# Performance work log

Measured on AMD Instinct MI355X. Metric: run time of the kernel, lower is better.

Reference implementation:

```python
import jax, jax.numpy as jnp
import numpy as np

B, C_IN, C_OUT, H, K = 64, 64, 128, 1855, 6


def setup_inputs() -> dict:
    key = jax.random.key(0)
    k1, k2, k3, k4 = jax.random.split(key, 4)
    x = jax.random.normal(k1, (B, C_IN, H), dtype=jnp.float32)
    # neighbor table [H, K]; valid indices first, -1 padding at the end
    neighbors = jax.random.randint(k2, (H, K), 0, H)
    n_boundary = H // 10
    neighbors = neighbors.at[:n_boundary, K - 2:].set(-1)
    weight_center = jax.random.normal(k3, (C_OUT, C_IN), dtype=jnp.float32) / np.sqrt(C_IN).astype(np.float32)
    weight_neighbors = jax.random.normal(k4, (C_OUT, C_IN, K), dtype=jnp.float32) / np.sqrt(C_IN * K).astype(np.float32)
    bias = jnp.zeros((C_OUT,), dtype=jnp.float32)
    return {
        "x": x,
        "neighbors": neighbors,
        "weight_center": weight_center,
        "weight_neighbors": weight_neighbors,
        "bias": bias,
    }


def reference(x, neighbors, weight_center, weight_neighbors, bias):
    # x: [B, C_in, H]; neighbors: [H, K] with -1 = invalid (valid-first ordering)
    mask = neighbors >= 0                               # [H, K]
    idx = jnp.where(mask, neighbors, 0)                 # safe gather indices
    gathered = x[:, :, idx] * mask.astype(x.dtype)[None, None, :, :]  # [B, C_in, H, K]
    center = jnp.einsum('bch,oc->boh', x, weight_center)              # [B, C_out, H]
    neigh = jnp.einsum('bchk,ock->boh', gathered, weight_neighbors)   # [B, C_out, H]
    counts = (1 + mask.sum(axis=-1)).astype(x.dtype)                  # [H]
    return (center + neigh) / counts[None, None, :] + bias[None, :, None]
```

## Files before the change

### kernel.cpp

```cpp
#include <hip/hip_runtime.h>
#include <stdint.h>

typedef __bf16 bf16x8 __attribute__((ext_vector_type(8)));
typedef float floatx4 __attribute__((ext_vector_type(4)));
typedef float floatx4u __attribute__((ext_vector_type(4), aligned(4)));
typedef unsigned int u32x4 __attribute__((ext_vector_type(4)));
typedef unsigned short u16;
typedef unsigned short u16x8 __attribute__((ext_vector_type(8)));
typedef unsigned int u32;

#define CIN   64
#define COUT  128
#define H_    1855
#define KNB   6
#define KTOT  448
#define NSTEPS 14

#define HROW   1040
#define HBUFSZ 16640

#define WP_OFF     ((size_t)H_ * 4096 * 2)
#define CINV_OFF   (WP_OFF + (size_t)COUT * KTOT * 2)
#define ZERO_OFF   (CINV_OFF + 7424)
#define SRCOFF_OFF (ZERO_OFF + 1024)
#define INVOFF 0xFFFFFFFFu

#define PIN4(v) asm volatile("" : "+v"(v))

typedef __attribute__((address_space(1))) unsigned int as1_u32;
typedef __attribute__((address_space(3))) unsigned int as3_u32;
static __device__ __forceinline__ void ld16_to_lds(const void* g, void* l) {
    __builtin_amdgcn_global_load_lds((const as1_u32*)g, (as3_u32*)l, 16, 0, 0);
}

static __device__ inline u16 f32_to_bf16(float f) {
    u32 u = __float_as_uint(f);
    u32 r = (u + 0x7FFFu + ((u >> 16) & 1u)) >> 16;
    return (u16)r;
}

__global__ __launch_bounds__(256) void k_prep(const float* __restrict__ x,
                                              const float* __restrict__ wc,
                                              const float* __restrict__ wn,
                                              const int* __restrict__ nbr,
                                              u16* __restrict__ xt3,
                                              u16* __restrict__ wp,
                                              float* __restrict__ cInvG,
                                              u32* __restrict__ zeroPg,
                                              u32* __restrict__ srcOff) {
    int tid = threadIdx.x;
    if (blockIdx.y == 64) {
        for (int tg = blockIdx.x * 256 + tid; tg < COUT * KTOT; tg += 29 * 256) {
            if (tg < 64) zeroPg[tg] = 0u;
            if (tg < H_) {
                int cnt = 1;
#pragma unroll
                for (int j = 0; j < KNB; ++j) cnt += (nbr[tg * KNB + j] >= 0) ? 1 : 0;
                cInvG[tg] = 1.0f / (float)cnt;
            }
            if (tg < H_ * 8) {
                int h = tg >> 3, s = tg & 7;
                u32 e;
                if (s == 0) e = (u32)h * 8192u;
                else if (s <= 6) {
                    int n = nbr[h * KNB + (s - 1)];
                    e = (n >= 0) ? (u32)n * 8192u : INVOFF;
                } else e = INVOFF;
                srcOff[tg] = e;
            }
            int o = tg / KTOT;
            int rem = tg - o * KTOT;
            int s = rem >> 6, c = rem & 63;
            float v = (s == 0) ? wc[o * CIN + c]
                               : wn[(o * CIN + c) * KNB + (s - 1)];
            wp[tg] = f32_to_bf16(v);
        }
        return;
    }
    __shared__ u16 tile[64][65];
    int h0  = blockIdx.x * 64;
    int bc0 = blockIdx.y * 64;
    int lh   = tid & 15;
    int rowi = tid >> 4;
    bool safe = (h0 + 64 <= H_);
#pragma unroll
    for (int i = 0; i < 4; ++i) {
        int row = i * 16 + rowi;
        int h = h0 + lh * 4;
        u16 v4[4];
        if (safe) {
            floatx4u f = *(const floatx4u*)(x + (size_t)(bc0 + row) * H_ + h);
#pragma unroll
            for (int j = 0; j < 4; ++j) v4[j] = f32_to_bf16(f[j]);
        } else {
#pragma unroll
            for (int j = 0; j < 4; ++j) {
                int hh = h + j;
                v4[j] = (hh < H_) ? f32_to_bf16(x[(size_t)(bc0 + row) * H_ + hh]) : (u16)0;
            }
        }
#pragma unroll
        for (int j = 0; j < 4; ++j) tile[row][lh * 4 + j] = v4[j];
    }
    __syncthreads();
    int bg = tid & 7;
    int hb = tid >> 3;
#pragma unroll
    for (int ii = 0; ii < 2; ++ii) {
        int hl = ii * 32 + hb;
        int hh = h0 + hl;
        u16x8 v;
#pragma unroll
        for (int j = 0; j < 8; ++j) v[j] = tile[bg * 8 + j][hl];
        if (hh < H_)
            *(u16x8*)(xt3 + (size_t)hh * 4096 + bc0 + bg * 8) = v;
    }
}

__global__ __launch_bounds__(256, 2) void k_main(const u16* __restrict__ xt3,
                                                 const u16* __restrict__ wp,
                                                 const float* __restrict__ bias,
                                                 const float* __restrict__ cInvG,
                                                 const u32* __restrict__ srcOff,
                                                 float* __restrict__ out) {
    __shared__ __align__(16) char LDS[4 * HBUFSZ];

    int tid  = threadIdx.x;
    int gbl  = blockIdx.x;
    int bp   = gbl & 31;
    int hs   = gbl >> 5;
    int b0   = bp * 2;
    int h0   = hs * 64;

    int lane = tid & 63;
    int wave = tid >> 6;
    int col  = lane & 15;
    int quad = lane >> 4;
    int m0w  = wave * 32;
    int lane16 = lane & 15;
    int ssub = lane >> 4;
    int bl   = lane16 >> 3;
    int chunk = lane16 & 7;

    const char* xb = (const char*)xt3;

    u32x4 afrag[2][NSTEPS];
#pragma unroll
    for (int mt = 0; mt < 2; ++mt) {
        int o = m0w + mt * 16 + col;
#pragma unroll
        for (int kk = 0; kk < NSTEPS; ++kk)
            afrag[mt][kk] = *(const u32x4*)(wp + o * KTOT + kk * 32 + quad * 8);
    }
#pragma unroll
    for (int mt = 0; mt < 2; ++mt)
#pragma unroll
        for (int kk = 0; kk < NSTEPS; ++kk)
            PIN4(afrag[mt][kk]);

    float biasv[2][4];
#pragma unroll
    for (int mt = 0; mt < 2; ++mt)
#pragma unroll
        for (int r = 0; r < 4; ++r)
            biasv[mt][r] = bias[m0w + mt * 16 + quad * 4 + r];

    float icv[4];
#pragma unroll
    for (int t = 0; t < 4; ++t) {
        int hic = h0 + t * 16 + col;
        icv[t] = cInvG[hic < H_ ? hic : 0];
    }

    u32 colOff = (u32)((b0 + bl) * 128 + chunk * 16);
    u32 zOff   = (u32)ZERO_OFF + (u32)(lane16 * 16);
    u32 offs[4][2][4];
#pragma unroll
    for (int t = 0; t < 4; ++t)
#pragma unroll
        for (int sg = 0; sg < 2; ++sg)
#pragma unroll
            for (int i = 0; i < 4; ++i) {
                int hh = h0 + t * 16 + wave * 4 + i;
                int s  = sg * 4 + ssub;
                u32 e = (hh < H_) ? srcOff[hh * 8 + s] : INVOFF;
                offs[t][sg][i] = (e == INVOFF) ? zOff : (e + colOff);
            }

    int rb0 = col * HROW + quad * 16;
    int rb1 = rb0 + 128;
    char* bufA0 = LDS;
    char* bufA1 = LDS + HBUFSZ;
    char* bufA2 = LDS + 2 * HBUFSZ;
    char* bufA3 = LDS + 3 * HBUFSZ;
    bool bnd = (hs == 28);

#define SGH(t, sg, bufp) do {                                                 \
    char* _d = (bufp) + (wave * 4) * HROW;                                    \
    _Pragma("unroll")                                                         \
    for (int _i = 0; _i < 4; ++_i)                                            \
        ld16_to_lds(xb + offs[t][sg][_i], _d + _i * HROW);                    \
} while (0)

#define CA(accv, bufp) do {                      \
    _Pragma("unroll") for (int _m = 0; _m < 2; ++_m)                          \
    _Pragma("unroll") for (int _n = 0; _n < 2; ++_n)                          \
        accv[_m][_n] = (floatx4){0.0f, 0.0f, 0.0f, 0.0f};                     \
    __builtin_amdgcn_s_setprio(1);                                            \
    _Pragma("unroll")                                                         \
    for (int kk = 0; kk < 8; ++kk) {                                          \
        int koff = (kk >> 1) * 256 + (kk & 1) * 64;                           \
        bf16x8 bfa = *(const bf16x8*)((bufp) + rb0 + koff);                   \
        bf16x8 bfb = *(const bf16x8*)((bufp) + rb1 + koff);                   \
        bf16x8 a0 = __builtin_bit_cast(bf16x8, afrag[0][kk]);                 \
        bf16x8 a1 = __builtin_bit_cast(bf16x8, afrag[1][kk]);                 \
        accv[0][0] = __builtin_amdgcn_mfma_f32_16x16x32_bf16(a0, bfa, accv[0][0], 0, 0, 0); \
        accv[1][0] = __builtin_amdgcn_mfma_f32_16x16x32_bf16(a1, bfa, accv[1][0], 0, 0, 0); \
        accv[0][1] = __builtin_amdgcn_mfma_f32_16x16x32_bf16(a0, bfb, accv[0][1], 0, 0, 0); \
        accv[1][1] = __builtin_amdgcn_mfma_f32_16x16x32_bf16(a1, bfb, accv[1][1], 0, 0, 0); \
    }                                                                         \
    __builtin_amdgcn_s_setprio(0);                                            \
} while (0)

#define CB(accv, bufp) do {                    \
    __builtin_amdgcn_s_setprio(1);                                            \
    _Pragma("unroll")                                                         \
    for (int kk = 8; kk < 14; ++kk) {                                         \
        int koff = ((kk - 8) >> 1) * 256 + (kk & 1) * 64;                     \
        bf16x8 bfa = *(const bf16x8*)((bufp) + rb0 + koff);                   \
        bf16x8 bfb = *(const bf16x8*)((bufp) + rb1 + koff);                   \
        bf16x8 a0 = __builtin_bit_cast(bf16x8, afrag[0][kk]);                 \
        bf16x8 a1 = __builtin_bit_cast(bf16x8, afrag[1][kk]);                 \
        accv[0][0] = __builtin_amdgcn_mfma_f32_16x16x32_bf16(a0, bfa, accv[0][0], 0, 0, 0); \
        accv[1][0] = __builtin_amdgcn_mfma_f32_16x16x32_bf16(a1, bfa, accv[1][0], 0, 0, 0); \
        accv[0][1] = __builtin_amdgcn_mfma_f32_16x16x32_bf16(a0, bfb, accv[0][1], 0, 0, 0); \
        accv[1][1] = __builtin_amdgcn_mfma_f32_16x16x32_bf16(a1, bfb, accv[1][1], 0, 0, 0); \
    }                                                                         \
    __builtin_amdgcn_s_setprio(0);                                            \
} while (0)

#define EPI(pp, a0v, a1v, Ebuf, BND) do {                                     \
    float* _E = (float*)((Ebuf) + (wave * 4) * HROW);                         \
    int _o8 = lane >> 3, _h4 = lane & 7;                                      \
    _Pragma("unroll")                                                         \
    for (int _nt = 0; _nt < 2; ++_nt) {                                       \
        asm volatile("s_waitcnt lgkmcnt(0)" ::: "memory");                    \
        _Pragma("unroll") for (int _mt = 0; _mt < 2; ++_mt)                   \
        _Pragma("unroll") for (int _r = 0; _r < 4; ++_r) {                    \
            int _ol = _mt * 16 + quad * 4 + _r;                               \
            int _x0 = ((col >> 2) ^ (_ol & 7));                               \
            int _x1 = (((16 + col) >> 2) ^ (_ol & 7));                        \
            _E[_ol * 32 + (_x0 << 2) + (col & 3)] =                           \
                a0v[_mt][_nt][_r] * icv[(pp) * 2]     + biasv[_mt][_r];       \
            _E[_ol * 32 + (_x1 << 2) + (col & 3)] =                           \
                a1v[_mt][_nt][_r] * icv[(pp) * 2 + 1] + biasv[_mt][_r];       \
        }                                                                     \
        asm volatile("s_waitcnt lgkmcnt(0)" ::: "memory");                    \
        _Pragma("unroll")                                                     \
        for (int _q = 0; _q < 4; ++_q) {                                      \
            int _ol = _q * 8 + _o8;                                           \
            floatx4 _v = *(const floatx4*)(_E + _ol * 32 + ((_h4 ^ (_ol & 7)) << 2)); \
            int _hh = h0 + (pp) * 32 + _h4 * 4;                               \
            float* _dst = out + (size_t)(b0 + _nt) * ((size_t)COUT * H_)      \
                        + (size_t)(m0w + _ol) * H_ + _hh;                     \
            if (!(BND)) {                                                     \
                *(floatx4u*)_dst = _v;                                        \
            } else {                                                          \
                _Pragma("unroll") for (int _e = 0; _e < 4; ++_e)              \
                    if (_hh + _e < H_) _dst[_e] = _v[_e];                     \
            }                                                                 \
        }                                                                     \
    }                                                                         \
} while (0)

#define VW(n)  asm volatile("s_waitcnt vmcnt(" #n ") lgkmcnt(0)" ::: "memory")
#define BAR()  __builtin_amdgcn_s_barrier()

    floatx4 acc0[2][2], acc1[2][2];

    SGH(0, 0, bufA0);
    SGH(0, 1, bufA1);
    SGH(1, 0, bufA2);

    VW(8);  BAR(); SGH(1, 1, bufA3);  CA(acc0, bufA0);
    VW(8);  BAR(); SGH(2, 0, bufA0);  CB(acc0, bufA1);
    VW(8);  BAR(); SGH(2, 1, bufA1);  CA(acc1, bufA2);
    VW(8);  BAR();                    CB(acc1, bufA3);
    EPI(0, acc0, acc1, bufA2, false);
    VW(12); BAR(); SGH(3, 0, bufA2);  CA(acc0, bufA0);
    VW(12); BAR(); SGH(3, 1, bufA3);  CB(acc0, bufA1);
    VW(4);  BAR();                    CA(acc1, bufA2);
    VW(0);  BAR();                    CB(acc1, bufA3);
    EPI(1, acc0, acc1, bufA2, bnd);

#undef SGH
#undef CA
#undef CB
#undef EPI
#undef VW
#undef BAR
}

extern "C" void kernel_launch(void* const* d_in, const int* in_sizes, int n_in,
                              void* d_out, int out_size, void* d_ws, size_t ws_size,
                              hipStream_t stream) {
    const float* x    = (const float*)d_in[0];
    const int*   nbr  = (const int*)d_in[1];
    const float* wc   = (const float*)d_in[2];
    const float* wn   = (const float*)d_in[3];
    const float* bias = (const float*)d_in[4];

    u16*   xt3    = (u16*)d_ws;
    u16*   wp     = (u16*)((char*)d_ws + WP_OFF);
    float* cInvG  = (float*)((char*)d_ws + CINV_OFF);
    u32*   zeroPg = (u32*)((char*)d_ws + ZERO_OFF);
    u32*   srcOff = (u32*)((char*)d_ws + SRCOFF_OFF);

    k_prep<<<dim3(29, 65), dim3(256), 0, stream>>>(
        x, wc, wn, nbr, xt3, wp, cInvG, zeroPg, srcOff);
    k_main<<<dim3(928), dim3(256), 0, stream>>>(
        xt3, wp, bias, cInvG, srcOff, (float*)d_out);
}
```

Measured before the change: 130.5 us.

## Halve LDS buffering for higher occupancy, write epilogue directly, pack prep transpose

The main kernel now uses two LDS gather buffers instead of four and raises the launch-bounds minimum to 4 blocks per SM, trading pipeline depth (waits now drain to vmcnt 0 at each step) for more resident waves. The epilogue drops its LDS-staged transpose and writes accumulator lanes straight to global memory, sending out-of-range tail writes to a dump buffer instead of branching. The prep transpose packs two bf16 rows per 32-bit LDS word so reads and stores are wider. The risks are less latency hiding per block and scattered, uncoalesced scalar output stores.

```diff
diff --git a/kernel.cpp b/kernel.cpp
--- a/kernel.cpp
+++ b/kernel.cpp
@@ -6,7 +6,6 @@
 typedef float floatx4u __attribute__((ext_vector_type(4), aligned(4)));
 typedef unsigned int u32x4 __attribute__((ext_vector_type(4)));
 typedef unsigned short u16;
-typedef unsigned short u16x8 __attribute__((ext_vector_type(8)));
 typedef unsigned int u32;
 
 #define CIN   64
@@ -23,6 +22,7 @@
 #define CINV_OFF   (WP_OFF + (size_t)COUT * KTOT * 2)
 #define ZERO_OFF   (CINV_OFF + 7424)
 #define SRCOFF_OFF (ZERO_OFF + 1024)
+#define DUMP_OFF   (SRCOFF_OFF + 59392)
 #define INVOFF 0xFFFFFFFFu
 
 #define PIN4(v) asm volatile("" : "+v"(v))
@@ -77,30 +77,36 @@
         }
         return;
     }
-    __shared__ u16 tile[64][65];
+    __shared__ u32 t32[64][34];
     int h0  = blockIdx.x * 64;
     int bc0 = blockIdx.y * 64;
-    int lh   = tid & 15;
-    int rowi = tid >> 4;
+    int lh = tid & 15;
+    int rq = tid >> 4;
     bool safe = (h0 + 64 <= H_);
 #pragma unroll
-    for (int i = 0; i < 4; ++i) {
-        int row = i * 16 + rowi;
+    for (int it = 0; it < 2; ++it) {
+        int rp = it * 16 + rq;
+        size_t r0 = (size_t)(bc0 + rp * 2) * H_;
+        size_t r1 = r0 + H_;
         int h = h0 + lh * 4;
-        u16 v4[4];
+        u32 p[4];
         if (safe) {
-            floatx4u f = *(const floatx4u*)(x + (size_t)(bc0 + row) * H_ + h);
-#pragma unroll
-            for (int j = 0; j < 4; ++j) v4[j] = f32_to_bf16(f[j]);
+            floatx4u f0 = *(const floatx4u*)(x + r0 + h);
+            floatx4u f1 = *(const floatx4u*)(x + r1 + h);
+#pragma unroll
+            for (int j = 0; j < 4; ++j)
+                p[j] = (u32)f32_to_bf16(f0[j]) | ((u32)f32_to_bf16(f1[j]) << 16);
         } else {
 #pragma unroll
             for (int j = 0; j < 4; ++j) {
                 int hh = h + j;
-                v4[j] = (hh < H_) ? f32_to_bf16(x[(size_t)(bc0 + row) * H_ + hh]) : (u16)0;
+                u16 a = 0, b = 0;
+                if (hh < H_) { a = f32_to_bf16(x[r0 + hh]); b = f32_to_bf16(x[r1 + hh]); }
+                p[j] = (u32)a | ((u32)b << 16);
             }
         }
 #pragma unroll
-        for (int j = 0; j < 4; ++j) tile[row][lh * 4 + j] = v4[j];
+        for (int j = 0; j < 4; ++j) t32[lh * 4 + j][rp] = p[j];
     }
     __syncthreads();
     int bg = tid & 7;
@@ -109,21 +115,22 @@
     for (int ii = 0; ii < 2; ++ii) {
         int hl = ii * 32 + hb;
         int hh = h0 + hl;
-        u16x8 v;
-#pragma unroll
-        for (int j = 0; j < 8; ++j) v[j] = tile[bg * 8 + j][hl];
+        uint2 qa = *(const uint2*)&t32[hl][bg * 4];
+        uint2 qb = *(const uint2*)&t32[hl][bg * 4 + 2];
+        u32x4 q = {qa.x, qa.y, qb.x, qb.y};
         if (hh < H_)
-            *(u16x8*)(xt3 + (size_t)hh * 4096 + bc0 + bg * 8) = v;
-    }
-}
-
-__global__ __launch_bounds__(256, 2) void k_main(const u16* __restrict__ xt3,
+            *(u32x4*)(xt3 + (size_t)hh * 4096 + bc0 + bg * 8) = q;
+    }
+}
+
+__global__ __launch_bounds__(256, 4) void k_main(const u16* __restrict__ xt3,
                                                  const u16* __restrict__ wp,
                                                  const float* __restrict__ bias,
                                                  const float* __restrict__ cInvG,
                                                  const u32* __restrict__ srcOff,
+                                                 float* __restrict__ dump,
                                                  float* __restrict__ out) {
-    __shared__ __align__(16) char LDS[4 * HBUFSZ];
+    __shared__ __align__(16) char LDS[2 * HBUFSZ];
 
     int tid  = threadIdx.x;
     int gbl  = blockIdx.x;
@@ -189,10 +196,8 @@
 
     int rb0 = col * HROW + quad * 16;
     int rb1 = rb0 + 128;
-    char* bufA0 = LDS;
-    char* bufA1 = LDS + HBUFSZ;
-    char* bufA2 = LDS + 2 * HBUFSZ;
-    char* bufA3 = LDS + 3 * HBUFSZ;
+    char* buf0 = LDS;
+    char* buf1 = LDS + HBUFSZ;
     bool bnd = (hs == 28);
 
 #define SGH(t, sg, bufp) do {                                                 \
@@ -239,37 +244,19 @@
     __builtin_amdgcn_s_setprio(0);                                            \
 } while (0)
 
-#define EPI(pp, a0v, a1v, Ebuf, BND) do {                                     \
-    float* _E = (float*)((Ebuf) + (wave * 4) * HROW);                         \
-    int _o8 = lane >> 3, _h4 = lane & 7;                                      \
-    _Pragma("unroll")                                                         \
-    for (int _nt = 0; _nt < 2; ++_nt) {                                       \
-        asm volatile("s_waitcnt lgkmcnt(0)" ::: "memory");                    \
-        _Pragma("unroll") for (int _mt = 0; _mt < 2; ++_mt)                   \
-        _Pragma("unroll") for (int _r = 0; _r < 4; ++_r) {                    \
-            int _ol = _mt * 16 + quad * 4 + _r;                               \
-            int _x0 = ((col >> 2) ^ (_ol & 7));                               \
-            int _x1 = (((16 + col) >> 2) ^ (_ol & 7));                        \
-            _E[_ol * 32 + (_x0 << 2) + (col & 3)] =                           \
-                a0v[_mt][_nt][_r] * icv[(pp) * 2]     + biasv[_mt][_r];       \
-            _E[_ol * 32 + (_x1 << 2) + (col & 3)] =                           \
-                a1v[_mt][_nt][_r] * icv[(pp) * 2 + 1] + biasv[_mt][_r];       \
-        }                                                                     \
-        asm volatile("s_waitcnt lgkmcnt(0)" ::: "memory");                    \
-        _Pragma("unroll")                                                     \
-        for (int _q = 0; _q < 4; ++_q) {                                      \
-            int _ol = _q * 8 + _o8;                                           \
-            floatx4 _v = *(const floatx4*)(_E + _ol * 32 + ((_h4 ^ (_ol & 7)) << 2)); \
-            int _hh = h0 + (pp) * 32 + _h4 * 4;                               \
-            float* _dst = out + (size_t)(b0 + _nt) * ((size_t)COUT * H_)      \
-                        + (size_t)(m0w + _ol) * H_ + _hh;                     \
-            if (!(BND)) {                                                     \
-                *(floatx4u*)_dst = _v;                                        \
-            } else {                                                          \
-                _Pragma("unroll") for (int _e = 0; _e < 4; ++_e)              \
-                    if (_hh + _e < H_) _dst[_e] = _v[_e];                     \
-            }                                                                 \
-        }                                                                     \
+#define EPI(pp, a0v, a1v, BND) do {                                           \
+    int _hl = h0 + (pp) * 32 + col;                                           \
+    float _il = icv[(pp) * 2], _ih = icv[(pp) * 2 + 1];                       \
+    _Pragma("unroll") for (int _nt = 0; _nt < 2; ++_nt)                       \
+    _Pragma("unroll") for (int _mt = 0; _mt < 2; ++_mt)                       \
+    _Pragma("unroll") for (int _r = 0; _r < 4; ++_r) {                        \
+        int _o = m0w + _mt * 16 + quad * 4 + _r;                              \
+        float* _d0 = out + (size_t)(b0 + _nt) * ((size_t)COUT * H_)           \
+                   + (size_t)_o * H_ + _hl;                                   \
+        float* _d1 = _d0 + 16;                                                \
+        if ((BND) && (_hl + 16 >= H_)) _d1 = dump + lane;                     \
+        *_d0 = a0v[_mt][_nt][_r] * _il + biasv[_mt][_r];                      \
+        *_d1 = a1v[_mt][_nt][_r] * _ih + biasv[_mt][_r];                      \
     }                                                                         \
 } while (0)
 
@@ -278,20 +265,17 @@
 
     floatx4 acc0[2][2], acc1[2][2];
 
-    SGH(0, 0, bufA0);
-    SGH(0, 1, bufA1);
-    SGH(1, 0, bufA2);
-
-    VW(8);  BAR(); SGH(1, 1, bufA3);  CA(acc0, bufA0);
-    VW(8);  BAR(); SGH(2, 0, bufA0);  CB(acc0, bufA1);
-    VW(8);  BAR(); SGH(2, 1, bufA1);  CA(acc1, bufA2);
-    VW(8);  BAR();                    CB(acc1, bufA3);
-    EPI(0, acc0, acc1, bufA2, false);
-    VW(12); BAR(); SGH(3, 0, bufA2);  CA(acc0, bufA0);
-    VW(12); BAR(); SGH(3, 1, bufA3);  CB(acc0, bufA1);
-    VW(4);  BAR();                    CA(acc1, bufA2);
-    VW(0);  BAR();                    CB(acc1, bufA3);
-    EPI(1, acc0, acc1, bufA2, bnd);
+    SGH(0, 0, buf0);
+    VW(0);  BAR(); SGH(0, 1, buf1); CA(acc0, buf0);
+    VW(0);  BAR(); SGH(1, 0, buf0); CB(acc0, buf1);
+    VW(0);  BAR(); SGH(1, 1, buf1); CA(acc1, buf0);
+    VW(0);  BAR(); SGH(2, 0, buf0); CB(acc1, buf1);
+    EPI(0, acc0, acc1, false);
+    VW(32); BAR(); SGH(2, 1, buf1); CA(acc0, buf0);
+    VW(0);  BAR(); SGH(3, 0, buf0); CB(acc0, buf1);
+    VW(0);  BAR(); SGH(3, 1, buf1); CA(acc1, buf0);
+    VW(0);  BAR();                  CB(acc1, buf1);
+    EPI(1, acc0, acc1, bnd);
 
 #undef SGH
 #undef CA
@@ -315,9 +299,10 @@
     float* cInvG  = (float*)((char*)d_ws + CINV_OFF);
     u32*   zeroPg = (u32*)((char*)d_ws + ZERO_OFF);
     u32*   srcOff = (u32*)((char*)d_ws + SRCOFF_OFF);
+    float* dump   = (float*)((char*)d_ws + DUMP_OFF);
 
     k_prep<<<dim3(29, 65), dim3(256), 0, stream>>>(
         x, wc, wn, nbr, xt3, wp, cInvG, zeroPg, srcOff);
     k_main<<<dim3(928), dim3(256), 0, stream>>>(
-        xt3, wp, bias, cInvG, srcOff, (float*)d_out);
-}
+        xt3, wp, bias, cInvG, srcOff, dump, (float*)d_out);
+}
```

Measured after the change: 220.2 us. 68.7% more time.

## Make main kernel persistent over two h-slices and pack bf16 pairs in transpose

Applied to the files above, without the earlier changes.

The main kernel now launches 512 blocks, and each block handles up to two h-slices in a loop. This amortizes the large register-resident weight fragment loads across more work and gives a single wave of blocks on 256 CUs at 2 blocks per CU. The prep transpose now packs two bf16 channel values into one u32 in shared memory, so it reads and writes wider words. The trade-off is load imbalance: blocks with slot 13-15 and the boundary slice do only one slice, and an extra barrier is added between slices.

```diff
diff --git a/kernel.cpp b/kernel.cpp
--- a/kernel.cpp
+++ b/kernel.cpp
@@ -6,7 +6,6 @@
 typedef float floatx4u __attribute__((ext_vector_type(4), aligned(4)));
 typedef unsigned int u32x4 __attribute__((ext_vector_type(4)));
 typedef unsigned short u16;
-typedef unsigned short u16x8 __attribute__((ext_vector_type(8)));
 typedef unsigned int u32;
 
 #define CIN   64
@@ -51,7 +50,7 @@
     int tid = threadIdx.x;
     if (blockIdx.y == 64) {
         for (int tg = blockIdx.x * 256 + tid; tg < COUT * KTOT; tg += 29 * 256) {
-            if (tg < 64) zeroPg[tg] = 0u;
+            if (tg < 128) zeroPg[tg] = 0u;
             if (tg < H_) {
                 int cnt = 1;
 #pragma unroll
@@ -77,30 +76,36 @@
         }
         return;
     }
-    __shared__ u16 tile[64][65];
+    __shared__ u32 t32[64][34];
     int h0  = blockIdx.x * 64;
     int bc0 = blockIdx.y * 64;
-    int lh   = tid & 15;
-    int rowi = tid >> 4;
+    int lh = tid & 15;
+    int rq = tid >> 4;
     bool safe = (h0 + 64 <= H_);
 #pragma unroll
-    for (int i = 0; i < 4; ++i) {
-        int row = i * 16 + rowi;
+    for (int it = 0; it < 2; ++it) {
+        int rp = it * 16 + rq;
+        size_t r0 = (size_t)(bc0 + rp * 2) * H_;
+        size_t r1 = r0 + H_;
         int h = h0 + lh * 4;
-        u16 v4[4];
+        u32 p[4];
         if (safe) {
-            floatx4u f = *(const floatx4u*)(x + (size_t)(bc0 + row) * H_ + h);
-#pragma unroll
-            for (int j = 0; j < 4; ++j) v4[j] = f32_to_bf16(f[j]);
+            floatx4u f0 = *(const floatx4u*)(x + r0 + h);
+            floatx4u f1 = *(const floatx4u*)(x + r1 + h);
+#pragma unroll
+            for (int j = 0; j < 4; ++j)
+                p[j] = (u32)f32_to_bf16(f0[j]) | ((u32)f32_to_bf16(f1[j]) << 16);
         } else {
 #pragma unroll
             for (int j = 0; j < 4; ++j) {
                 int hh = h + j;
-                v4[j] = (hh < H_) ? f32_to_bf16(x[(size_t)(bc0 + row) * H_ + hh]) : (u16)0;
+                u16 a = 0, b = 0;
+                if (hh < H_) { a = f32_to_bf16(x[r0 + hh]); b = f32_to_bf16(x[r1 + hh]); }
+                p[j] = (u32)a | ((u32)b << 16);
             }
         }
 #pragma unroll
-        for (int j = 0; j < 4; ++j) tile[row][lh * 4 + j] = v4[j];
+        for (int j = 0; j < 4; ++j) t32[lh * 4 + j][rp] = p[j];
     }
     __syncthreads();
     int bg = tid & 7;
@@ -109,11 +114,11 @@
     for (int ii = 0; ii < 2; ++ii) {
         int hl = ii * 32 + hb;
         int hh = h0 + hl;
-        u16x8 v;
-#pragma unroll
-        for (int j = 0; j < 8; ++j) v[j] = tile[bg * 8 + j][hl];
+        uint2 qa = *(const uint2*)&t32[hl][bg * 4];
+        uint2 qb = *(const uint2*)&t32[hl][bg * 4 + 2];
+        u32x4 q = {qa.x, qa.y, qb.x, qb.y};
         if (hh < H_)
-            *(u16x8*)(xt3 + (size_t)hh * 4096 + bc0 + bg * 8) = v;
+            *(u32x4*)(xt3 + (size_t)hh * 4096 + bc0 + bg * 8) = q;
     }
 }
 
@@ -128,9 +133,8 @@
     int tid  = threadIdx.x;
     int gbl  = blockIdx.x;
     int bp   = gbl & 31;
-    int hs   = gbl >> 5;
+    int slot = gbl >> 5;
     int b0   = bp * 2;
-    int h0   = hs * 64;
 
     int lane = tid & 63;
     int wave = tid >> 6;
@@ -165,27 +169,8 @@
         for (int r = 0; r < 4; ++r)
             biasv[mt][r] = bias[m0w + mt * 16 + quad * 4 + r];
 
-    float icv[4];
-#pragma unroll
-    for (int t = 0; t < 4; ++t) {
-        int hic = h0 + t * 16 + col;
-        icv[t] = cInvG[hic < H_ ? hic : 0];
-    }
-
     u32 colOff = (u32)((b0 + bl) * 128 + chunk * 16);
     u32 zOff   = (u32)ZERO_OFF + (u32)(lane16 * 16);
-    u32 offs[4][2][4];
-#pragma unroll
-    for (int t = 0; t < 4; ++t)
-#pragma unroll
-        for (int sg = 0; sg < 2; ++sg)
-#pragma unroll
-            for (int i = 0; i < 4; ++i) {
-                int hh = h0 + t * 16 + wave * 4 + i;
-                int s  = sg * 4 + ssub;
-                u32 e = (hh < H_) ? srcOff[hh * 8 + s] : INVOFF;
-                offs[t][sg][i] = (e == INVOFF) ? zOff : (e + colOff);
-            }
 
     int rb0 = col * HROW + quad * 16;
     int rb1 = rb0 + 128;
@@ -193,7 +178,6 @@
     char* bufA1 = LDS + HBUFSZ;
     char* bufA2 = LDS + 2 * HBUFSZ;
     char* bufA3 = LDS + 3 * HBUFSZ;
-    bool bnd = (hs == 28);
 
 #define SGH(t, sg, bufp) do {                                                 \
     char* _d = (bufp) + (wave * 4) * HROW;                                    \
@@ -277,21 +261,49 @@
 #define BAR()  __builtin_amdgcn_s_barrier()
 
     floatx4 acc0[2][2], acc1[2][2];
-
-    SGH(0, 0, bufA0);
-    SGH(0, 1, bufA1);
-    SGH(1, 0, bufA2);
-
-    VW(8);  BAR(); SGH(1, 1, bufA3);  CA(acc0, bufA0);
-    VW(8);  BAR(); SGH(2, 0, bufA0);  CB(acc0, bufA1);
-    VW(8);  BAR(); SGH(2, 1, bufA1);  CA(acc1, bufA2);
-    VW(8);  BAR();                    CB(acc1, bufA3);
-    EPI(0, acc0, acc1, bufA2, false);
-    VW(12); BAR(); SGH(3, 0, bufA2);  CA(acc0, bufA0);
-    VW(12); BAR(); SGH(3, 1, bufA3);  CB(acc0, bufA1);
-    VW(4);  BAR();                    CA(acc1, bufA2);
-    VW(0);  BAR();                    CB(acc1, bufA3);
-    EPI(1, acc0, acc1, bufA2, bnd);
+    int nhs = (slot + 16 <= 28) ? 2 : 1;
+
+    for (int q = 0; q < nhs; ++q) {
+        int hs = slot + q * 16;
+        int h0 = hs * 64;
+        bool bnd = (hs == 28);
+
+        float icv[4];
+#pragma unroll
+        for (int t = 0; t < 4; ++t) {
+            int hic = h0 + t * 16 + col;
+            icv[t] = cInvG[hic < H_ ? hic : 0];
+        }
+        u32 offs[4][2][4];
+#pragma unroll
+        for (int t = 0; t < 4; ++t)
+#pragma unroll
+            for (int sg = 0; sg < 2; ++sg)
+#pragma unroll
+                for (int i = 0; i < 4; ++i) {
+                    int hh = h0 + t * 16 + wave * 4 + i;
+                    int s  = sg * 4 + ssub;
+                    u32 e = (hh < H_) ? srcOff[hh * 8 + s] : INVOFF;
+                    offs[t][sg][i] = (e == INVOFF) ? zOff : (e + colOff);
+                }
+
+        SGH(0, 0, bufA0);
+        SGH(0, 1, bufA1);
+        SGH(1, 0, bufA2);
+
+        VW(8);  BAR(); SGH(1, 1, bufA3);  CA(acc0, bufA0);
+        VW(8);  BAR(); SGH(2, 0, bufA0);  CB(acc0, bufA1);
+        VW(8);  BAR(); SGH(2, 1, bufA1);  CA(acc1, bufA2);
+        VW(8);  BAR();                    CB(acc1, bufA3);
+        EPI(0, acc0, acc1, bufA2, false);
+        VW(12); BAR(); SGH(3, 0, bufA2);  CA(acc0, bufA0);
+        VW(12); BAR(); SGH(3, 1, bufA3);  CB(acc0, bufA1);
+        VW(4);  BAR();                    CA(acc1, bufA2);
+        VW(0);  BAR();                    CB(acc1, bufA3);
+        EPI(1, acc0, acc1, bufA2, bnd);
+
+        if (q + 1 < nhs) { VW(0); BAR(); }
+    }
 
 #undef SGH
 #undef CA
@@ -318,6 +330,6 @@
 
     k_prep<<<dim3(29, 65), dim3(256), 0, stream>>>(
         x, wc, wn, nbr, xt3, wp, cInvG, zeroPg, srcOff);
-    k_main<<<dim3(928), dim3(256), 0, stream>>>(
+    k_main<<<dim3(512), dim3(256), 0, stream>>>(
         xt3, wp, bias, cInvG, srcOff, (float*)d_out);
 }
```

Result: faster. 126.6 us (-3.0%).
